# Performance work log

Hardware: AMD Instinct MI355X
Metric: run time of the kernel (lower is better)

The kernel has to match this reference:

```python
import jax, jax.numpy as jnp
import numpy as np

N, F_IN, F_HID, F_OUT, E = 100000, 128, 256, 40, 1600000
LOG_SQRT_2PI = 0.9189385332046727  # log(sqrt(2*pi))


def setup_inputs() -> dict:
    key = jax.random.key(0)
    ks = jax.random.split(key, 12)
    s_in = 1.0 / np.sqrt(F_IN)
    s_hid = 1.0 / np.sqrt(F_HID)
    s_out = 1.0 / np.sqrt(F_OUT)
    return {
        "x": jax.random.normal(ks[0], (N, F_IN), jnp.float32),
        "adj_row": jax.random.randint(ks[1], (E,), 0, N, jnp.int32),
        "adj_col": jax.random.randint(ks[2], (E,), 0, N, jnp.int32),
        "adj_val": jax.random.uniform(ks[3], (E,), jnp.float32) * 0.1,
        "eps": jax.random.normal(ks[4], (1, N, F_IN), jnp.float32),
        "Wz1": jax.random.normal(ks[5], (F_IN, F_IN), jnp.float32) * s_in,
        "bz1": jnp.zeros((F_IN,), jnp.float32),
        "Wz2": jax.random.normal(ks[6], (F_IN, 2 * F_IN), jnp.float32) * s_in,
        "bz2": jnp.zeros((2 * F_IN,), jnp.float32),
        "W0": jax.random.uniform(ks[7], (F_IN, F_HID), jnp.float32, -s_hid, s_hid),
        "b0": jax.random.uniform(ks[8], (F_HID,), jnp.float32, -s_hid, s_hid),
        "W1": jax.random.uniform(ks[9], (F_HID, F_OUT), jnp.float32, -s_out, s_out),
        "b1": jax.random.uniform(ks[10], (F_OUT,), jnp.float32, -s_out, s_out),
    }


def spmm(row, col, val, mat):
    # sparse [N,N] (COO) @ dense [N,D] -> [N,D] via gather + segment_sum
    return jax.ops.segment_sum(val[:, None] * mat[col], row, num_segments=mat.shape[0])


def reference(x, adj_row, adj_col, adj_val, eps, Wz1, bz1, Wz2, bz2, W0, b0, W1, b1):
    # z_w MLP: Linear -> ReLU -> Linear producing [N, 2*F_IN]
    feats = jax.nn.relu(x @ Wz1 + bz1) @ Wz2 + bz2
    z_x_hat = spmm(adj_row, adj_col, adj_val, feats)  # [N, 2*F_IN]
    mean = z_x_hat[:, :F_IN]
    std = jax.nn.softplus(z_x_hat[:, F_IN:]) + 0.01
    # rsample((1,)): [1, N, F_IN]
    z = mean[None] + std[None] * eps
    # diagonal Normal log-probs, summed over feature dim
    logq = (-0.5 * ((z - mean[None]) / std[None]) ** 2 - jnp.log(std)[None] - LOG_SQRT_2PI).sum(-1)
    logp = (-0.5 * z ** 2 - LOG_SQRT_2PI).sum(-1)
    l2 = (logq - logp).mean(0).mean()
    h = z.mean(0)  # [N, F_IN]
    # GCN layer 1: dense transform then spmm, relu (dropout off in eval)
    h = jax.nn.relu(spmm(adj_row, adj_col, adj_val, h @ W0) + b0)
    # GCN layer 2 (output)
    out = spmm(adj_row, adj_col, adj_val, h @ W1) + b1
    return jax.nn.log_softmax(out, axis=1), l2
```

## Files before the change

kernel.cpp:

```cpp
#include <hip/hip_runtime.h>
#include <math.h>

constexpr int NN = 100000;
constexpr int NCHUNK = 128;
constexpr int RROWS  = 12500;

using f32x4 = __attribute__((ext_vector_type(4))) float;
using s16x8 = __attribute__((ext_vector_type(8))) short;
using us8   = __attribute__((ext_vector_type(8))) unsigned short;
using us4   = __attribute__((ext_vector_type(4))) unsigned short;

__device__ __forceinline__ unsigned short f2bf(float f) {
    unsigned u = __float_as_uint(f);
    unsigned r = u + 0x7FFFu + ((u >> 16) & 1u);
    return (unsigned short)(r >> 16);
}
__device__ __forceinline__ float bf2f(unsigned short u) {
    return __uint_as_float(((unsigned)u) << 16);
}

__device__ __forceinline__ void wfrag_body(
    const float* __restrict__ W, short* __restrict__ Wf,
    int K, int NC, int tid)
{
    const int KK = K / 32;
    int lane = tid & 63, f = tid >> 6;
    int ncg = f / KK, kk = f % KK;
    int col = ncg * 16 + (lane & 15);
    int k0  = kk * 32 + 8 * (lane >> 4);
    s16x8 o;
    #pragma unroll
    for (int j = 0; j < 8; ++j)
        o[j] = (col < NC) ? (short)f2bf(W[(size_t)(k0 + j) * NC + col]) : (short)0;
    *reinterpret_cast<s16x8*>(Wf + (size_t)tid * 8) = o;
}

__global__ __launch_bounds__(256) void wfrag_all(
    const float* __restrict__ Wz1, const float* __restrict__ Wz2,
    const float* __restrict__ W0,  const float* __restrict__ W1,
    short* wz1f, short* wz2f, short* w0f, short* w1f)
{
    int b = blockIdx.x;
    if (b < 8)       wfrag_body(Wz1, wz1f, 128, 128, b * 256 + threadIdx.x);
    else if (b < 24) wfrag_body(Wz2, wz2f, 128, 256, (b - 8) * 256 + threadIdx.x);
    else if (b < 40) wfrag_body(W0,  w0f,  128, 256, (b - 24) * 256 + threadIdx.x);
    else {
        int tid = (b - 40) * 256 + threadIdx.x;
        if (tid < 3 * 8 * 64) wfrag_body(W1, w1f, 256, 40, tid);
    }
}

template<int K, int WM, int WN, int CB, int AK, bool OBF16, int BIASMODE, bool ORELU>
__global__ __launch_bounds__(WM * WN * 64) void gemm_mfma(
    const void* __restrict__ Ain, const short* __restrict__ Wf,
    const float* __restrict__ bias, const float* __restrict__ b0,
    void* __restrict__ Cout, int M, int NCout)
{
    constexpr int KK = K / 32;
    const int tid = threadIdx.x;
    const int lane = tid & 63, wid = tid >> 6;
    const int wm = wid % WM, wn = wid / WM;
    const int rowBase = blockIdx.x * (WM * 64) + wm * 64;
    const int cfb = wn * CB;
    const int l15 = lane & 15, lh = lane >> 4;

    f32x4 acc[4][CB];
    #pragma unroll
    for (int i = 0; i < 4; ++i)
        #pragma unroll
        for (int j = 0; j < CB; ++j) acc[i][j] = (f32x4)0.f;

    #pragma unroll
    for (int kk = 0; kk < KK; ++kk) {
        const int k0 = kk * 32 + lh * 8;
        s16x8 a[4];
        #pragma unroll
        for (int rb = 0; rb < 4; ++rb) {
            int row = rowBase + rb * 16 + l15;
            row = row < M ? row : M - 1;
            if (AK == 0) {
                const float* ap = (const float*)Ain + (size_t)row * K + k0;
                float4 u = *reinterpret_cast<const float4*>(ap);
                float4 v = *reinterpret_cast<const float4*>(ap + 4);
                a[rb][0] = (short)f2bf(u.x); a[rb][1] = (short)f2bf(u.y);
                a[rb][2] = (short)f2bf(u.z); a[rb][3] = (short)f2bf(u.w);
                a[rb][4] = (short)f2bf(v.x); a[rb][5] = (short)f2bf(v.y);
                a[rb][6] = (short)f2bf(v.z); a[rb][7] = (short)f2bf(v.w);
            } else if (AK == 1) {
                a[rb] = *reinterpret_cast<const s16x8*>((const short*)Ain + (size_t)row * K + k0);
            } else {
                s16x8 s = *reinterpret_cast<const s16x8*>((const short*)Ain + (size_t)row * K + k0);
                float4 ba = *reinterpret_cast<const float4*>(b0 + k0);
                float4 bb = *reinterpret_cast<const float4*>(b0 + k0 + 4);
                float bv[8] = {ba.x, ba.y, ba.z, ba.w, bb.x, bb.y, bb.z, bb.w};
                #pragma unroll
                for (int j = 0; j < 8; ++j) {
                    float fv = bf2f((unsigned short)s[j]) + bv[j];
                    a[rb][j] = (short)f2bf(fmaxf(fv, 0.f));
                }
            }
        }
        s16x8 b[CB];
        #pragma unroll
        for (int cb = 0; cb < CB; ++cb)
            b[cb] = *reinterpret_cast<const s16x8*>(
                Wf + ((size_t)((cfb + cb) * KK + kk) * 64 + lane) * 8);
        #pragma unroll
        for (int rb = 0; rb < 4; ++rb)
            #pragma unroll
            for (int cb = 0; cb < CB; ++cb)
                acc[rb][cb] = __builtin_amdgcn_mfma_f32_16x16x32_bf16(
                    a[rb], b[cb], acc[rb][cb], 0, 0, 0);
    }

    #pragma unroll
    for (int cb = 0; cb < CB; ++cb) {
        int col = (cfb + cb) * 16 + l15;
        if (col >= NCout) continue;
        float bs = (BIASMODE != 0) ? bias[col] : 0.f;
        #pragma unroll
        for (int rb = 0; rb < 4; ++rb) {
            #pragma unroll
            for (int r = 0; r < 4; ++r) {
                int row = rowBase + rb * 16 + lh * 4 + r;
                if (row >= M) continue;
                float v = acc[rb][cb][r];
                if (BIASMODE == 1) v += bs;
                if (ORELU) v = fmaxf(v, 0.f);
                if (OBF16)
                    ((unsigned short*)Cout)[(size_t)row * NCout + col] = f2bf(v);
                else
                    ((float*)Cout)[(size_t)row * NCout + col] = v;
            }
        }
    }
}

__global__ __launch_bounds__(256) void gemm_z_sample(
    const unsigned short* __restrict__ A, const short* __restrict__ Wf,
    const float* __restrict__ bz2, const float* __restrict__ rowsum,
    const float* __restrict__ eps, unsigned short* __restrict__ hout,
    float* __restrict__ partials)
{
    const int tid = threadIdx.x;
    const int lane = tid & 63, wid = tid >> 6;
    const int rowBase = blockIdx.x * 64;
    const int l15 = lane & 15, lh = lane >> 4;

    const int cf[4] = {wid * 2, wid * 2 + 1, 8 + wid * 2, 8 + wid * 2 + 1};

    f32x4 acc[4][4];
    #pragma unroll
    for (int i = 0; i < 4; ++i)
        #pragma unroll
        for (int j = 0; j < 4; ++j) acc[i][j] = (f32x4)0.f;

    #pragma unroll
    for (int kk = 0; kk < 4; ++kk) {
        const int k0 = kk * 32 + lh * 8;
        s16x8 a[4];
        #pragma unroll
        for (int rb = 0; rb < 4; ++rb) {
            int row = rowBase + rb * 16 + l15;
            row = row < NN ? row : NN - 1;
            a[rb] = *reinterpret_cast<const s16x8*>(A + (size_t)row * 128 + k0);
        }
        s16x8 b[4];
        #pragma unroll
        for (int cb = 0; cb < 4; ++cb)
            b[cb] = *reinterpret_cast<const s16x8*>(
                Wf + ((size_t)(cf[cb] * 4 + kk) * 64 + lane) * 8);
        #pragma unroll
        for (int rb = 0; rb < 4; ++rb)
            #pragma unroll
            for (int cb = 0; cb < 4; ++cb)
                acc[rb][cb] = __builtin_amdgcn_mfma_f32_16x16x32_bf16(
                    a[rb], b[cb], acc[rb][cb], 0, 0, 0);
    }

    const float bsm0 = bz2[wid * 32 + l15];
    const float bsm1 = bz2[wid * 32 + 16 + l15];
    const float bss0 = bz2[128 + wid * 32 + l15];
    const float bss1 = bz2[128 + wid * 32 + 16 + l15];
    float p = 0.f;
    #pragma unroll
    for (int rb = 0; rb < 4; ++rb) {
        #pragma unroll
        for (int r = 0; r < 4; ++r) {
            int row = rowBase + rb * 16 + lh * 4 + r;
            if (row >= NN) continue;
            float rs = rowsum[row];
            #pragma unroll
            for (int cb = 0; cb < 2; ++cb) {
                int colm = wid * 32 + cb * 16 + l15;
                float mean = acc[rb][cb][r]     + rs * (cb ? bsm1 : bsm0);
                float sv   = acc[rb][2 + cb][r] + rs * (cb ? bss1 : bss0);
                float sp = fmaxf(sv, 0.f) + log1pf(expf(-fabsf(sv)));
                float sd = sp + 0.01f;
                float e  = eps[(size_t)row * 128 + colm];
                float h  = mean + sd * e;
                hout[(size_t)row * 128 + colm] = f2bf(h);
                p += 0.5f * h * h - 0.5f * e * e - logf(sd);
            }
        }
    }
    #pragma unroll
    for (int o = 32; o > 0; o >>= 1) p += __shfl_xor(p, o);
    __shared__ float ws[4];
    if (lane == 0) ws[wid] = p;
    __syncthreads();
    if (tid == 0) partials[blockIdx.x] = ws[0] + ws[1] + ws[2] + ws[3];
}

__global__ __launch_bounds__(256) void hist_part(
    const int* __restrict__ row, unsigned short* __restrict__ part, int E, int chunkE)
{
    __shared__ unsigned lcnt[RROWS / 2];
    const int chunk = blockIdx.x;
    const int rowLo = blockIdx.y * RROWS;
    for (int i = threadIdx.x; i < RROWS / 2; i += 256) lcnt[i] = 0u;
    __syncthreads();
    const int e0 = chunk * chunkE;
    const int e1 = min(e0 + chunkE, E);
    for (int e = e0 + threadIdx.x; e < e1; e += 256) {
        int lr = row[e] - rowLo;
        if ((unsigned)lr < (unsigned)RROWS)
            atomicAdd(&lcnt[lr >> 1], 1u << ((lr & 1) << 4));
    }
    __syncthreads();
    unsigned* dst = reinterpret_cast<unsigned*>(part + (size_t)chunk * NN + rowLo);
    for (int i = threadIdx.x; i < RROWS / 2; i += 256) dst[i] = lcnt[i];
}

__global__ __launch_bounds__(256) void chunk_scan(
    unsigned short* __restrict__ part, int* __restrict__ cnt)
{
    int r = blockIdx.x * 256 + threadIdx.x;
    if (r >= NN) return;
    int run = 0;
    for (int c0 = 0; c0 < NCHUNK; c0 += 8) {
        int v[8];
        #pragma unroll
        for (int j = 0; j < 8; ++j) v[j] = part[(size_t)(c0 + j) * NN + r];
        #pragma unroll
        for (int j = 0; j < 8; ++j) {
            part[(size_t)(c0 + j) * NN + r] = (unsigned short)run;
            run += v[j];
        }
    }
    cnt[r] = run;
}

__global__ __launch_bounds__(256) void scan_blk(
    const int* __restrict__ cnt, int* __restrict__ rp, int* __restrict__ bsums, int n)
{
    const int t = threadIdx.x;
    const int lane = t & 63, wid = t >> 6;
    const int base = blockIdx.x * 1024 + t * 4;
    int a0 = 0, a1 = 0, a2 = 0, a3 = 0;
    if (base + 3 < n) {
        int4 v = *reinterpret_cast<const int4*>(&cnt[base]);
        a0 = v.x; a1 = v.y; a2 = v.z; a3 = v.w;
    } else {
        if (base + 0 < n) a0 = cnt[base + 0];
        if (base + 1 < n) a1 = cnt[base + 1];
        if (base + 2 < n) a2 = cnt[base + 2];
        if (base + 3 < n) a3 = cnt[base + 3];
    }
    int s0 = a0, s1 = s0 + a1, s2 = s1 + a2, s3 = s2 + a3;
    int v = s3;
    #pragma unroll
    for (int o = 1; o < 64; o <<= 1) {
        int u = __shfl_up(v, o);
        if (lane >= o) v += u;
    }
    __shared__ int wtot[4];
    if (lane == 63) wtot[wid] = v;
    __syncthreads();
    int woff = 0;
    #pragma unroll
    for (int w = 0; w < 4; ++w) if (w < wid) woff += wtot[w];
    int texcl = woff + v - s3;
    if (base + 0 < n) rp[base + 0] = texcl;
    if (base + 1 < n) rp[base + 1] = texcl + s0;
    if (base + 2 < n) rp[base + 2] = texcl + s1;
    if (base + 3 < n) rp[base + 3] = texcl + s2;
    if (t == 255) bsums[blockIdx.x] = woff + v;
}

__global__ void scan_mid(const int* __restrict__ bsums, int* __restrict__ boff, int nb)
{
    if (threadIdx.x == 0 && blockIdx.x == 0) {
        int run = 0;
        for (int b = 0; b < nb; ++b) { boff[b] = run; run += bsums[b]; }
    }
}

__global__ __launch_bounds__(256) void scan_add(
    int* __restrict__ rp, const int* __restrict__ boff, int n, int E)
{
    int i = blockIdx.x * 256 + threadIdx.x;
    if (i < n) rp[i] += boff[i >> 10];
    if (i == 0) rp[n] = E;
}

__global__ __launch_bounds__(256) void scatter_part(
    const int* __restrict__ row, const int* __restrict__ col,
    const float* __restrict__ val, const int* __restrict__ rp,
    const unsigned short* __restrict__ part, int2* __restrict__ edges,
    int E, int chunkE)
{
    __shared__ unsigned lcnt[RROWS / 2];
    const int chunk = blockIdx.x;
    const int rowLo = blockIdx.y * RROWS;
    for (int i = threadIdx.x; i < RROWS / 2; i += 256) lcnt[i] = 0u;
    __syncthreads();
    const int e0 = chunk * chunkE;
    const int e1 = min(e0 + chunkE, E);
    const unsigned short* choff = part + (size_t)chunk * NN;
    for (int e = e0 + threadIdx.x; e < e1; e += 256) {
        int r = row[e];
        int lr = r - rowLo;
        if ((unsigned)lr < (unsigned)RROWS) {
            unsigned old = atomicAdd(&lcnt[lr >> 1], 1u << ((lr & 1) << 4));
            int local = (int)((old >> ((lr & 1) << 4)) & 0xFFFFu);
            int p = rp[r] + (int)choff[r] + local;
            edges[p] = make_int2(col[e], __float_as_int(val[e]));
        }
    }
}

template<bool RS>
__global__ __launch_bounds__(256) void spmm128(
    const int* __restrict__ rp, const int2* __restrict__ edges,
    const unsigned short* __restrict__ mat, unsigned short* __restrict__ out,
    float* __restrict__ rowsum)
{
    int gid = blockIdx.x * 256 + threadIdx.x;
    int r = gid >> 4, sl = gid & 15;
    if (r >= NN) return;
    const int beg = rp[r], end = rp[r + 1];
    float acc[8] = {};
    float vs = 0.f;
    int e = beg;
    for (; e + 7 < end; e += 8) {
        int2 c[8]; float v[8]; us8 f[8];
        #pragma unroll
        for (int k = 0; k < 8; ++k) c[k] = edges[e + k];
        #pragma unroll
        for (int k = 0; k < 8; ++k) {
            v[k] = __int_as_float(c[k].y);
            f[k] = *reinterpret_cast<const us8*>(mat + (size_t)c[k].x * 128 + sl * 8);
        }
        if (RS) vs += v[0] + v[1] + v[2] + v[3] + v[4] + v[5] + v[6] + v[7];
        #pragma unroll
        for (int k = 0; k < 8; ++k)
            #pragma unroll
            for (int j = 0; j < 8; ++j) acc[j] += v[k] * bf2f(f[k][j]);
    }
    for (; e + 3 < end; e += 4) {
        int2 c[4]; float v[4]; us8 f[4];
        #pragma unroll
        for (int k = 0; k < 4; ++k) c[k] = edges[e + k];
        #pragma unroll
        for (int k = 0; k < 4; ++k) {
            v[k] = __int_as_float(c[k].y);
            f[k] = *reinterpret_cast<const us8*>(mat + (size_t)c[k].x * 128 + sl * 8);
        }
        if (RS) vs += v[0] + v[1] + v[2] + v[3];
        #pragma unroll
        for (int k = 0; k < 4; ++k)
            #pragma unroll
            for (int j = 0; j < 8; ++j) acc[j] += v[k] * bf2f(f[k][j]);
    }
    for (; e < end; ++e) {
        int2 cv = edges[e];
        float v = __int_as_float(cv.y);
        if (RS) vs += v;
        us8 f = *reinterpret_cast<const us8*>(mat + (size_t)cv.x * 128 + sl * 8);
        #pragma unroll
        for (int j = 0; j < 8; ++j) acc[j] += v * bf2f(f[j]);
    }
    us8 o;
    #pragma unroll
    for (int j = 0; j < 8; ++j) o[j] = f2bf(acc[j]);
    *reinterpret_cast<us8*>(out + (size_t)r * 128 + sl * 8) = o;
    if (RS && sl == 0) rowsum[r] = vs;
}

__global__ __launch_bounds__(256) void spmm40_lsm(
    const int* __restrict__ rp, const int2* __restrict__ edges,
    const unsigned short* __restrict__ mat, const float* __restrict__ b1,
    float* __restrict__ out)
{
    int gid = blockIdx.x * 256 + threadIdx.x;
    int r = gid >> 4, sl = gid & 15;
    const int beg = rp[r], end = rp[r + 1];
    float4 acc = make_float4(0.f, 0.f, 0.f, 0.f);
    int e = beg;
    for (; e + 3 < end; e += 4) {
        int2 c[4];
        #pragma unroll
        for (int k = 0; k < 4; ++k) c[k] = edges[e + k];
        if (sl < 10) {
            #pragma unroll
            for (int k = 0; k < 4; ++k) {
                float v = __int_as_float(c[k].y);
                us4 m = *reinterpret_cast<const us4*>(mat + (size_t)c[k].x * 40 + sl * 4);
                acc.x += v * bf2f(m[0]); acc.y += v * bf2f(m[1]);
                acc.z += v * bf2f(m[2]); acc.w += v * bf2f(m[3]);
            }
        }
    }
    for (; e < end; ++e) {
        int2 cv = edges[e];
        float v = __int_as_float(cv.y);
        if (sl < 10) {
            us4 m = *reinterpret_cast<const us4*>(mat + (size_t)cv.x * 40 + sl * 4);
            acc.x += v * bf2f(m[0]); acc.y += v * bf2f(m[1]);
            acc.z += v * bf2f(m[2]); acc.w += v * bf2f(m[3]);
        }
    }
    float xv[4] = {-1e30f, -1e30f, -1e30f, -1e30f};
    if (sl < 10) {
        xv[0] = acc.x + b1[sl * 4 + 0]; xv[1] = acc.y + b1[sl * 4 + 1];
        xv[2] = acc.z + b1[sl * 4 + 2]; xv[3] = acc.w + b1[sl * 4 + 3];
    }
    float m = fmaxf(fmaxf(xv[0], xv[1]), fmaxf(xv[2], xv[3]));
    #pragma unroll
    for (int o = 1; o < 16; o <<= 1) m = fmaxf(m, __shfl_xor(m, o, 16));
    float ssum = 0.f;
    #pragma unroll
    for (int k = 0; k < 4; ++k) ssum += (sl < 10) ? expf(xv[k] - m) : 0.f;
    #pragma unroll
    for (int o = 1; o < 16; o <<= 1) ssum += __shfl_xor(ssum, o, 16);
    if (sl < 10) {
        float lse = m + logf(ssum);
        float4 o4 = make_float4(xv[0] - lse, xv[1] - lse, xv[2] - lse, xv[3] - lse);
        *reinterpret_cast<float4*>(out + (size_t)r * 40 + sl * 4) = o4;
    }
}

__global__ __launch_bounds__(256) void finalize_l2(
    const float* __restrict__ partials, int np, float* __restrict__ out)
{
    double a = 0.0;
    for (int i = threadIdx.x; i < np; i += 256) a += (double)partials[i];
    #pragma unroll
    for (int o = 32; o > 0; o >>= 1) a += __shfl_xor(a, o);
    __shared__ double ws[4];
    if ((threadIdx.x & 63) == 0) ws[threadIdx.x >> 6] = a;
    __syncthreads();
    if (threadIdx.x == 0)
        out[(size_t)NN * 40] = (float)((ws[0] + ws[1] + ws[2] + ws[3]) / (double)NN);
}

extern "C" void kernel_launch(void* const* d_in, const int* in_sizes, int n_in,
                              void* d_out, int out_size, void* d_ws, size_t ws_size,
                              hipStream_t stream)
{
    const float* x    = (const float*)d_in[0];
    const int*   arow = (const int*)d_in[1];
    const int*   acol = (const int*)d_in[2];
    const float* aval = (const float*)d_in[3];
    const float* eps  = (const float*)d_in[4];
    const float* Wz1  = (const float*)d_in[5];
    const float* bz1  = (const float*)d_in[6];
    const float* Wz2  = (const float*)d_in[7];
    const float* bz2  = (const float*)d_in[8];
    const float* W0   = (const float*)d_in[9];
    const float* b0   = (const float*)d_in[10];
    const float* W1   = (const float*)d_in[11];
    const float* b1   = (const float*)d_in[12];
    float* out = (float*)d_out;
    const int E = in_sizes[1];

    char* p = (char*)d_ws;
    auto alloc = [&](size_t bytes) {
        char* q = p;
        p += (bytes + 15) & ~(size_t)15;
        return (void*)q;
    };
    int2* edges           = (int2*)alloc((size_t)E * 8);
    unsigned short* part  = (unsigned short*)alloc((size_t)NCHUNK * NN * 2);
    int*  rp              = (int*)alloc((size_t)(NN + 4) * 4);
    int*  cnt             = (int*)alloc((size_t)NN * 4);
    float* rowsum         = (float*)alloc((size_t)NN * 4);
    int*  bsums           = (int*)alloc(128 * 4);
    int*  boff            = (int*)alloc(128 * 4);
    float* partials       = (float*)alloc(1568 * 4);
    unsigned short* bufT  = (unsigned short*)alloc((size_t)NN * 128 * 2);
    unsigned short* bufU  = (unsigned short*)alloc((size_t)NN * 128 * 2);
    unsigned short* bufZ  = (unsigned short*)alloc((size_t)NN * 256 * 2);
    short* wz1f           = (short*)alloc(8  * 4 * 64 * 8 * 2);
    short* wz2f           = (short*)alloc(16 * 4 * 64 * 8 * 2);
    short* w0f            = (short*)alloc(16 * 4 * 64 * 8 * 2);
    short* w1f            = (short*)alloc(3  * 8 * 64 * 8 * 2);

    dim3 blk(256);
    const int nScan = (NN + 1023) / 1024;
    const int gSp = (NN * 16) / 256;
    const int chunkE = (E + NCHUNK - 1) / NCHUNK;
    const dim3 gPart(NCHUNK, NN / RROWS);

    wfrag_all<<<dim3(46), blk, 0, stream>>>(Wz1, Wz2, W0, W1, wz1f, wz2f, w0f, w1f);

    hist_part<<<gPart, blk, 0, stream>>>(arow, part, E, chunkE);
    chunk_scan<<<dim3((NN + 255) / 256), blk, 0, stream>>>(part, cnt);
    scan_blk<<<dim3(nScan), blk, 0, stream>>>(cnt, rp, bsums, NN);
    scan_mid<<<dim3(1), dim3(64), 0, stream>>>(bsums, boff, nScan);
    scan_add<<<dim3((NN + 256) / 256), blk, 0, stream>>>(rp, boff, NN, E);
    scatter_part<<<gPart, blk, 0, stream>>>(arow, acol, aval, rp, part, edges, E, chunkE);

    gemm_mfma<128, 2, 2, 4, 0, true, 1, true><<<dim3(782), blk, 0, stream>>>(
        x, wz1f, bz1, nullptr, bufT, NN, 128);
    spmm128<true><<<dim3(gSp), blk, 0, stream>>>(rp, edges, bufT, bufU, rowsum);
    gemm_z_sample<<<dim3(1563), blk, 0, stream>>>(bufU, wz2f, bz2, rowsum, eps, bufU, partials);
    spmm128<false><<<dim3(gSp), blk, 0, stream>>>(rp, edges, bufU, bufT, nullptr);
    gemm_mfma<128, 1, 4, 4, 1, true, 0, false><<<dim3(1563), blk, 0, stream>>>(
        bufT, w0f, nullptr, nullptr, bufZ, NN, 256);
    gemm_mfma<256, 4, 1, 3, 2, true, 0, false><<<dim3(391), blk, 0, stream>>>(
        bufZ, w1f, nullptr, b0, bufT, NN, 40);
    spmm40_lsm<<<dim3(gSp), blk, 0, stream>>>(rp, edges, bufT, b1, out);
    finalize_l2<<<dim3(1), blk, 0, stream>>>(partials, 1563, out);
}
```

Measured before the change: 491.7 us.

## Sort rows by degree for SpMM load balance and use fast math intrinsics

Adds a degree-bucketing pass (histogram, scan, scatter) that builds a row permutation so each SpMM wavefront processes rows of similar degree. This is meant to reduce lane divergence from the variable-length edge loops in the three SpMM kernels. It also swaps expf, logf and log1pf for the fast __expf/__logf intrinsics in the sampling and log-softmax epilogues. The cost is four extra small launches plus a memset, an indirection through perm that scatters output writes, and slightly lower accuracy in softplus for small values.

```diff
diff --git a/kernel.cpp b/kernel.cpp
--- a/kernel.cpp
+++ b/kernel.cpp
@@ -195,12 +195,13 @@
                 int colm = wid * 32 + cb * 16 + l15;
                 float mean = acc[rb][cb][r]     + rs * (cb ? bsm1 : bsm0);
                 float sv   = acc[rb][2 + cb][r] + rs * (cb ? bss1 : bss0);
-                float sp = fmaxf(sv, 0.f) + log1pf(expf(-fabsf(sv)));
+                float ea = __expf(-fabsf(sv));
+                float sp = fmaxf(sv, 0.f) + __logf(1.f + ea);
                 float sd = sp + 0.01f;
                 float e  = eps[(size_t)row * 128 + colm];
                 float h  = mean + sd * e;
                 hout[(size_t)row * 128 + colm] = f2bf(h);
-                p += 0.5f * h * h - 0.5f * e * e - logf(sd);
+                p += 0.5f * h * h - 0.5f * e * e - __logf(sd);
             }
         }
     }
@@ -330,15 +331,54 @@
     }
 }
 
+__global__ __launch_bounds__(256) void deg_hist(
+    const int* __restrict__ rp, int* __restrict__ bins)
+{
+    __shared__ int lh[64];
+    if (threadIdx.x < 64) lh[threadIdx.x] = 0;
+    __syncthreads();
+    int r = blockIdx.x * 256 + threadIdx.x;
+    if (r < NN) atomicAdd(&lh[min(rp[r + 1] - rp[r], 63)], 1);
+    __syncthreads();
+    if (threadIdx.x < 64 && lh[threadIdx.x]) atomicAdd(&bins[threadIdx.x], lh[threadIdx.x]);
+}
+
+__global__ void bin_scan(const int* __restrict__ bins, int* __restrict__ cursor)
+{
+    if (threadIdx.x == 0 && blockIdx.x == 0) {
+        int run = 0;
+        for (int i = 0; i < 64; ++i) { cursor[i] = run; run += bins[i]; }
+    }
+}
+
+__global__ __launch_bounds__(256) void deg_scatter(
+    const int* __restrict__ rp, int* __restrict__ cursor, int* __restrict__ perm)
+{
+    __shared__ int lh[64], lbase[64];
+    if (threadIdx.x < 64) lh[threadIdx.x] = 0;
+    __syncthreads();
+    int r = blockIdx.x * 256 + threadIdx.x;
+    int d = 0, lpos = 0;
+    if (r < NN) {
+        d = min(rp[r + 1] - rp[r], 63);
+        lpos = atomicAdd(&lh[d], 1);
+    }
+    __syncthreads();
+    if (threadIdx.x < 64)
+        lbase[threadIdx.x] = lh[threadIdx.x] ? atomicAdd(&cursor[threadIdx.x], lh[threadIdx.x]) : 0;
+    __syncthreads();
+    if (r < NN) perm[lbase[d] + lpos] = r;
+}
+
 template<bool RS>
 __global__ __launch_bounds__(256) void spmm128(
-    const int* __restrict__ rp, const int2* __restrict__ edges,
+    const int* __restrict__ rp, const int* __restrict__ perm,
+    const int2* __restrict__ edges,
     const unsigned short* __restrict__ mat, unsigned short* __restrict__ out,
     float* __restrict__ rowsum)
 {
     int gid = blockIdx.x * 256 + threadIdx.x;
-    int r = gid >> 4, sl = gid & 15;
-    if (r >= NN) return;
+    int r = perm[gid >> 4], sl = gid & 15;
     const int beg = rp[r], end = rp[r + 1];
     float acc[8] = {};
     float vs = 0.f;
@@ -389,12 +429,13 @@
 }
 
 __global__ __launch_bounds__(256) void spmm40_lsm(
-    const int* __restrict__ rp, const int2* __restrict__ edges,
+    const int* __restrict__ rp, const int* __restrict__ perm,
+    const int2* __restrict__ edges,
     const unsigned short* __restrict__ mat, const float* __restrict__ b1,
     float* __restrict__ out)
 {
     int gid = blockIdx.x * 256 + threadIdx.x;
-    int r = gid >> 4, sl = gid & 15;
+    int r = perm[gid >> 4], sl = gid & 15;
     const int beg = rp[r], end = rp[r + 1];
     float4 acc = make_float4(0.f, 0.f, 0.f, 0.f);
     int e = beg;
@@ -431,11 +472,11 @@
     for (int o = 1; o < 16; o <<= 1) m = fmaxf(m, __shfl_xor(m, o, 16));
     float ssum = 0.f;
     #pragma unroll
-    for (int k = 0; k < 4; ++k) ssum += (sl < 10) ? expf(xv[k] - m) : 0.f;
+    for (int k = 0; k < 4; ++k) ssum += (sl < 10) ? __expf(xv[k] - m) : 0.f;
     #pragma unroll
     for (int o = 1; o < 16; o <<= 1) ssum += __shfl_xor(ssum, o, 16);
     if (sl < 10) {
-        float lse = m + logf(ssum);
+        float lse = m + __logf(ssum);
         float4 o4 = make_float4(xv[0] - lse, xv[1] - lse, xv[2] - lse, xv[3] - lse);
         *reinterpret_cast<float4*>(out + (size_t)r * 40 + sl * 4) = o4;
     }
@@ -488,6 +529,9 @@
     float* rowsum         = (float*)alloc((size_t)NN * 4);
     int*  bsums           = (int*)alloc(128 * 4);
     int*  boff            = (int*)alloc(128 * 4);
+    int*  bins            = (int*)alloc(64 * 4);
+    int*  cursor          = (int*)alloc(64 * 4);
+    int*  perm            = (int*)alloc((size_t)NN * 4);
     float* partials       = (float*)alloc(1568 * 4);
     unsigned short* bufT  = (unsigned short*)alloc((size_t)NN * 128 * 2);
     unsigned short* bufU  = (unsigned short*)alloc((size_t)NN * 128 * 2);
@@ -500,27 +544,33 @@
     dim3 blk(256);
     const int nScan = (NN + 1023) / 1024;
     const int gSp = (NN * 16) / 256;
+    const int gN  = (NN + 255) / 256;
     const int chunkE = (E + NCHUNK - 1) / NCHUNK;
     const dim3 gPart(NCHUNK, NN / RROWS);
 
     wfrag_all<<<dim3(46), blk, 0, stream>>>(Wz1, Wz2, W0, W1, wz1f, wz2f, w0f, w1f);
 
     hist_part<<<gPart, blk, 0, stream>>>(arow, part, E, chunkE);
-    chunk_scan<<<dim3((NN + 255) / 256), blk, 0, stream>>>(part, cnt);
+    chunk_scan<<<dim3(gN), blk, 0, stream>>>(part, cnt);
     scan_blk<<<dim3(nScan), blk, 0, stream>>>(cnt, rp, bsums, NN);
     scan_mid<<<dim3(1), dim3(64), 0, stream>>>(bsums, boff, nScan);
     scan_add<<<dim3((NN + 256) / 256), blk, 0, stream>>>(rp, boff, NN, E);
     scatter_part<<<gPart, blk, 0, stream>>>(arow, acol, aval, rp, part, edges, E, chunkE);
 
+    hipMemsetAsync(bins, 0, 64 * sizeof(int), stream);
+    deg_hist<<<dim3(gN), blk, 0, stream>>>(rp, bins);
+    bin_scan<<<dim3(1), dim3(64), 0, stream>>>(bins, cursor);
+    deg_scatter<<<dim3(gN), blk, 0, stream>>>(rp, cursor, perm);
+
     gemm_mfma<128, 2, 2, 4, 0, true, 1, true><<<dim3(782), blk, 0, stream>>>(
         x, wz1f, bz1, nullptr, bufT, NN, 128);
-    spmm128<true><<<dim3(gSp), blk, 0, stream>>>(rp, edges, bufT, bufU, rowsum);
+    spmm128<true><<<dim3(gSp), blk, 0, stream>>>(rp, perm, edges, bufT, bufU, rowsum);
     gemm_z_sample<<<dim3(1563), blk, 0, stream>>>(bufU, wz2f, bz2, rowsum, eps, bufU, partials);
-    spmm128<false><<<dim3(gSp), blk, 0, stream>>>(rp, edges, bufU, bufT, nullptr);
+    spmm128<false><<<dim3(gSp), blk, 0, stream>>>(rp, perm, edges, bufU, bufT, nullptr);
     gemm_mfma<128, 1, 4, 4, 1, true, 0, false><<<dim3(1563), blk, 0, stream>>>(
         bufT, w0f, nullptr, nullptr, bufZ, NN, 256);
     gemm_mfma<256, 4, 1, 3, 2, true, 0, false><<<dim3(391), blk, 0, stream>>>(
         bufZ, w1f, nullptr, b0, bufT, NN, 40);
-    spmm40_lsm<<<dim3(gSp), blk, 0, stream>>>(rp, edges, bufT, b1, out);
+    spmm40_lsm<<<dim3(gSp), blk, 0, stream>>>(rp, perm, edges, bufT, b1, out);
     finalize_l2<<<dim3(1), blk, 0, stream>>>(partials, 1563, out);
 }
```

Result: no change. 489.4 us (-0.5%).

## Fuse SpMM gathers into the following MFMA GEMMs via LDS tiles

Applied to the files above, without the earlier changes.

Each 128-wide SpMM is merged with the GEMM that consumes it. The gathered row aggregates go into a swizzled LDS tile, and MFMA reads its A fragments from that tile. This drops the global write and re-read of the intermediate [N,128] buffers and the rowsum array, and removes two kernel launches. It also swaps exp/log for the fast __expf/__logf intrinsics in the sampling and log-softmax epilogues. The trade-offs are lower occupancy from the LDS use, a gather loop unrolled 4-wide instead of 8-wide, and possible imbalance from varying row degrees inside a block.

```diff
diff --git a/kernel.cpp b/kernel.cpp
--- a/kernel.cpp
+++ b/kernel.cpp
@@ -136,19 +136,79 @@
     }
 }
 
-__global__ __launch_bounds__(256) void gemm_z_sample(
-    const unsigned short* __restrict__ A, const short* __restrict__ Wf,
-    const float* __restrict__ bz2, const float* __restrict__ rowsum,
-    const float* __restrict__ eps, unsigned short* __restrict__ hout,
-    float* __restrict__ partials)
-{
+__device__ __forceinline__ void gather_tile(
+    const int* __restrict__ rp, const int2* __restrict__ edges,
+    const unsigned short* __restrict__ mat, int rowBase,
+    unsigned short* Als, float* rsls, bool wantRS)
+{
+    const int t = threadIdx.x;
+    const int g = t >> 4, sl = t & 15;
+    #pragma unroll
+    for (int it = 0; it < 4; ++it) {
+        int lr = g * 4 + it;
+        int row = rowBase + lr;
+        float acc[8] = {};
+        float vs = 0.f;
+        if (row < NN) {
+            int e = rp[row];
+            const int end = rp[row + 1];
+            for (; e + 3 < end; e += 4) {
+                int2 c[4]; float v[4]; us8 f[4];
+                #pragma unroll
+                for (int k = 0; k < 4; ++k) c[k] = edges[e + k];
+                #pragma unroll
+                for (int k = 0; k < 4; ++k) {
+                    v[k] = __int_as_float(c[k].y);
+                    f[k] = *reinterpret_cast<const us8*>(mat + (size_t)c[k].x * 128 + sl * 8);
+                }
+                vs += v[0] + v[1] + v[2] + v[3];
+                #pragma unroll
+                for (int k = 0; k < 4; ++k)
+                    #pragma unroll
+                    for (int j = 0; j < 8; ++j) acc[j] += v[k] * bf2f(f[k][j]);
+            }
+            for (; e < end; ++e) {
+                int2 cv = edges[e];
+                float v = __int_as_float(cv.y);
+                vs += v;
+                us8 f = *reinterpret_cast<const us8*>(mat + (size_t)cv.x * 128 + sl * 8);
+                #pragma unroll
+                for (int j = 0; j < 8; ++j) acc[j] += v * bf2f(f[j]);
+            }
+        }
+        us8 o;
+        #pragma unroll
+        for (int j = 0; j < 8; ++j) o[j] = f2bf(acc[j]);
+        unsigned byteoff = (unsigned)(lr * 256 + ((sl * 16) ^ ((lr & 7) << 4)));
+        *reinterpret_cast<us8*>((char*)Als + byteoff) = o;
+        if (wantRS && sl == 0) rsls[lr] = vs;
+    }
+}
+
+__device__ __forceinline__ s16x8 lds_afrag(const unsigned short* Als, int lrow, int k0)
+{
+    unsigned byteoff = (unsigned)(lrow * 256 + (((k0 * 2) & 255) ^ ((lrow & 7) << 4)));
+    return *reinterpret_cast<const s16x8*>((const char*)Als + byteoff);
+}
+
+__global__ __launch_bounds__(256) void spmm_gemm_z_sample(
+    const int* __restrict__ rp, const int2* __restrict__ edges,
+    const unsigned short* __restrict__ t1, const short* __restrict__ Wf,
+    const float* __restrict__ bz2, const float* __restrict__ eps,
+    unsigned short* __restrict__ hout, float* __restrict__ partials)
+{
+    __shared__ unsigned short Als[64 * 128];
+    __shared__ float rsls[64];
+    __shared__ float ws[4];
     const int tid = threadIdx.x;
     const int lane = tid & 63, wid = tid >> 6;
     const int rowBase = blockIdx.x * 64;
     const int l15 = lane & 15, lh = lane >> 4;
 
+    gather_tile(rp, edges, t1, rowBase, Als, rsls, true);
+    __syncthreads();
+
     const int cf[4] = {wid * 2, wid * 2 + 1, 8 + wid * 2, 8 + wid * 2 + 1};
-
     f32x4 acc[4][4];
     #pragma unroll
     for (int i = 0; i < 4; ++i)
@@ -160,11 +220,8 @@
         const int k0 = kk * 32 + lh * 8;
         s16x8 a[4];
         #pragma unroll
-        for (int rb = 0; rb < 4; ++rb) {
-            int row = rowBase + rb * 16 + l15;
-            row = row < NN ? row : NN - 1;
-            a[rb] = *reinterpret_cast<const s16x8*>(A + (size_t)row * 128 + k0);
-        }
+        for (int rb = 0; rb < 4; ++rb)
+            a[rb] = lds_afrag(Als, rb * 16 + l15, k0);
         s16x8 b[4];
         #pragma unroll
         for (int cb = 0; cb < 4; ++cb)
@@ -187,29 +244,86 @@
     for (int rb = 0; rb < 4; ++rb) {
         #pragma unroll
         for (int r = 0; r < 4; ++r) {
-            int row = rowBase + rb * 16 + lh * 4 + r;
+            int lrow = rb * 16 + lh * 4 + r;
+            int row = rowBase + lrow;
             if (row >= NN) continue;
-            float rs = rowsum[row];
+            float rs = rsls[lrow];
             #pragma unroll
             for (int cb = 0; cb < 2; ++cb) {
                 int colm = wid * 32 + cb * 16 + l15;
                 float mean = acc[rb][cb][r]     + rs * (cb ? bsm1 : bsm0);
                 float sv   = acc[rb][2 + cb][r] + rs * (cb ? bss1 : bss0);
-                float sp = fmaxf(sv, 0.f) + log1pf(expf(-fabsf(sv)));
+                float ea = __expf(-fabsf(sv));
+                float sp = fmaxf(sv, 0.f) + __logf(1.f + ea);
                 float sd = sp + 0.01f;
                 float e  = eps[(size_t)row * 128 + colm];
                 float h  = mean + sd * e;
                 hout[(size_t)row * 128 + colm] = f2bf(h);
-                p += 0.5f * h * h - 0.5f * e * e - logf(sd);
+                p += 0.5f * h * h - 0.5f * e * e - __logf(sd);
             }
         }
     }
     #pragma unroll
     for (int o = 32; o > 0; o >>= 1) p += __shfl_xor(p, o);
-    __shared__ float ws[4];
     if (lane == 0) ws[wid] = p;
     __syncthreads();
     if (tid == 0) partials[blockIdx.x] = ws[0] + ws[1] + ws[2] + ws[3];
+}
+
+__global__ __launch_bounds__(256) void spmm_gemm256(
+    const int* __restrict__ rp, const int2* __restrict__ edges,
+    const unsigned short* __restrict__ h, const short* __restrict__ Wf,
+    unsigned short* __restrict__ s2out)
+{
+    __shared__ unsigned short Als[64 * 128];
+    const int tid = threadIdx.x;
+    const int lane = tid & 63, wid = tid >> 6;
+    const int rowBase = blockIdx.x * 64;
+    const int l15 = lane & 15, lh = lane >> 4;
+
+    gather_tile(rp, edges, h, rowBase, Als, nullptr, false);
+    __syncthreads();
+
+    const int cfb = wid * 4;
+    f32x4 acc[4][4];
+    #pragma unroll
+    for (int i = 0; i < 4; ++i)
+        #pragma unroll
+        for (int j = 0; j < 4; ++j) acc[i][j] = (f32x4)0.f;
+
+    #pragma unroll
+    for (int kk = 0; kk < 4; ++kk) {
+        const int k0 = kk * 32 + lh * 8;
+        s16x8 a[4];
+        #pragma unroll
+        for (int rb = 0; rb < 4; ++rb)
+            a[rb] = lds_afrag(Als, rb * 16 + l15, k0);
+        s16x8 b[4];
+        #pragma unroll
+        for (int cb = 0; cb < 4; ++cb)
+            b[cb] = *reinterpret_cast<const s16x8*>(
+                Wf + ((size_t)((cfb + cb) * 4 + kk) * 64 + lane) * 8);
+        #pragma unroll
+        for (int rb = 0; rb < 4; ++rb)
+            #pragma unroll
+            for (int cb = 0; cb < 4; ++cb)
+                acc[rb][cb] = __builtin_amdgcn_mfma_f32_16x16x32_bf16(
+                    a[rb], b[cb], acc[rb][cb], 0, 0, 0);
+    }
+
+    #pragma unroll
+    for (int cb = 0; cb < 4; ++cb) {
+        int col = (cfb + cb) * 16 + l15;
+        #pragma unroll
+        for (int rb = 0; rb < 4; ++rb) {
+            #pragma unroll
+            for (int r = 0; r < 4; ++r) {
+                int row = rowBase + rb * 16 + lh * 4 + r;
+                if (row >= NN) continue;
+                s2out[(size_t)row * 256 + col] = f2bf(acc[rb][cb][r]);
+            }
+        }
+    }
 }
 
 __global__ __launch_bounds__(256) void hist_part(
@@ -330,64 +444,6 @@
     }
 }
 
-template<bool RS>
-__global__ __launch_bounds__(256) void spmm128(
-    const int* __restrict__ rp, const int2* __restrict__ edges,
-    const unsigned short* __restrict__ mat, unsigned short* __restrict__ out,
-    float* __restrict__ rowsum)
-{
-    int gid = blockIdx.x * 256 + threadIdx.x;
-    int r = gid >> 4, sl = gid & 15;
-    if (r >= NN) return;
-    const int beg = rp[r], end = rp[r + 1];
-    float acc[8] = {};
-    float vs = 0.f;
-    int e = beg;
-    for (; e + 7 < end; e += 8) {
-        int2 c[8]; float v[8]; us8 f[8];
-        #pragma unroll
-        for (int k = 0; k < 8; ++k) c[k] = edges[e + k];
-        #pragma unroll
-        for (int k = 0; k < 8; ++k) {
-            v[k] = __int_as_float(c[k].y);
-            f[k] = *reinterpret_cast<const us8*>(mat + (size_t)c[k].x * 128 + sl * 8);
-        }
-        if (RS) vs += v[0] + v[1] + v[2] + v[3] + v[4] + v[5] + v[6] + v[7];
-        #pragma unroll
-        for (int k = 0; k < 8; ++k)
-            #pragma unroll
-            for (int j = 0; j < 8; ++j) acc[j] += v[k] * bf2f(f[k][j]);
-    }
-    for (; e + 3 < end; e += 4) {
-        int2 c[4]; float v[4]; us8 f[4];
-        #pragma unroll
-        for (int k = 0; k < 4; ++k) c[k] = edges[e + k];
-        #pragma unroll
-        for (int k = 0; k < 4; ++k) {
-            v[k] = __int_as_float(c[k].y);
-            f[k] = *reinterpret_cast<const us8*>(mat + (size_t)c[k].x * 128 + sl * 8);
-        }
-        if (RS) vs += v[0] + v[1] + v[2] + v[3];
-        #pragma unroll
-        for (int k = 0; k < 4; ++k)
-            #pragma unroll
-            for (int j = 0; j < 8; ++j) acc[j] += v[k] * bf2f(f[k][j]);
-    }
-    for (; e < end; ++e) {
-        int2 cv = edges[e];
-        float v = __int_as_float(cv.y);
-        if (RS) vs += v;
-        us8 f = *reinterpret_cast<const us8*>(mat + (size_t)cv.x * 128 + sl * 8);
-        #pragma unroll
-        for (int j = 0; j < 8; ++j) acc[j] += v * bf2f(f[j]);
-    }
-    us8 o;
-    #pragma unroll
-    for (int j = 0; j < 8; ++j) o[j] = f2bf(acc[j]);
-    *reinterpret_cast<us8*>(out + (size_t)r * 128 + sl * 8) = o;
-    if (RS && sl == 0) rowsum[r] = vs;
-}
-
 __global__ __launch_bounds__(256) void spmm40_lsm(
     const int* __restrict__ rp, const int2* __restrict__ edges,
     const unsigned short* __restrict__ mat, const float* __restrict__ b1,
@@ -431,11 +487,11 @@
     for (int o = 1; o < 16; o <<= 1) m = fmaxf(m, __shfl_xor(m, o, 16));
     float ssum = 0.f;
     #pragma unroll
-    for (int k = 0; k < 4; ++k) ssum += (sl < 10) ? expf(xv[k] - m) : 0.f;
+    for (int k = 0; k < 4; ++k) ssum += (sl < 10) ? __expf(xv[k] - m) : 0.f;
     #pragma unroll
     for (int o = 1; o < 16; o <<= 1) ssum += __shfl_xor(ssum, o, 16);
     if (sl < 10) {
-        float lse = m + logf(ssum);
+        float lse = m + __logf(ssum);
         float4 o4 = make_float4(xv[0] - lse, xv[1] - lse, xv[2] - lse, xv[3] - lse);
         *reinterpret_cast<float4*>(out + (size_t)r * 40 + sl * 4) = o4;
     }
@@ -485,7 +541,6 @@
     unsigned short* part  = (unsigned short*)alloc((size_t)NCHUNK * NN * 2);
     int*  rp              = (int*)alloc((size_t)(NN + 4) * 4);
     int*  cnt             = (int*)alloc((size_t)NN * 4);
-    float* rowsum         = (float*)alloc((size_t)NN * 4);
     int*  bsums           = (int*)alloc(128 * 4);
     int*  boff            = (int*)alloc(128 * 4);
     float* partials       = (float*)alloc(1568 * 4);
@@ -500,6 +555,7 @@
     dim3 blk(256);
     const int nScan = (NN + 1023) / 1024;
     const int gSp = (NN * 16) / 256;
+    const int gF  = (NN + 63) / 64;
     const int chunkE = (E + NCHUNK - 1) / NCHUNK;
     const dim3 gPart(NCHUNK, NN / RROWS);
 
@@ -514,13 +570,11 @@
 
     gemm_mfma<128, 2, 2, 4, 0, true, 1, true><<<dim3(782), blk, 0, stream>>>(
         x, wz1f, bz1, nullptr, bufT, NN, 128);
-    spmm128<true><<<dim3(gSp), blk, 0, stream>>>(rp, edges, bufT, bufU, rowsum);
-    gemm_z_sample<<<dim3(1563), blk, 0, stream>>>(bufU, wz2f, bz2, rowsum, eps, bufU, partials);
-    spmm128<false><<<dim3(gSp), blk, 0, stream>>>(rp, edges, bufU, bufT, nullptr);
-    gemm_mfma<128, 1, 4, 4, 1, true, 0, false><<<dim3(1563), blk, 0, stream>>>(
-        bufT, w0f, nullptr, nullptr, bufZ, NN, 256);
+    spmm_gemm_z_sample<<<dim3(gF), blk, 0, stream>>>(
+        rp, edges, bufT, wz2f, bz2, eps, bufU, partials);
+    spmm_gemm256<<<dim3(gF), blk, 0, stream>>>(rp, edges, bufU, w0f, bufZ);
     gemm_mfma<256, 4, 1, 3, 2, true, 0, false><<<dim3(391), blk, 0, stream>>>(
         bufZ, w1f, nullptr, b0, bufT, NN, 40);
     spmm40_lsm<<<dim3(gSp), blk, 0, stream>>>(rp, edges, bufT, b1, out);
-    finalize_l2<<<dim3(1), blk, 0, stream>>>(partials, 1563, out);
-}
+    finalize_l2<<<dim3(1), blk, 0, stream>>>(partials, gF, out);
+}
```

Measured after the change: 470.4 us. 4.3% less time.
